# Performance work log

Measured on AMD Instinct MI355X. Metric: run time of the kernel, lower is better.

## Reference

```python
import jax, jax.numpy as jnp
import numpy as np

B, C, LO, LQ, H = 64, 4, 64, 128, 768
NEG = -10000.0


def _trilinear(u, um, v, vm, w1, b1, w2, b2, w3):
    # u: [N, Lu, H], v: [N, Lv, H]; returns [N, Lu, Lv]
    p1 = u @ w1 + b1                                  # [N, Lu, 1]
    p2 = (v @ w2 + b2).transpose(0, 2, 1)             # [N, 1, Lv]
    p3 = jnp.einsum('bud,bvd->buv', u * w3, v)        # trilinear term
    return p1 + p2 + p3 + ((1.0 - um) * NEG)[:, :, None] + ((1.0 - vm) * NEG)[:, None, :]


def _forward(encoded_o, encoded_q, om, qm,
             att_W1_w, att_W1_b, att_W2_w, att_W2_b, att_W3,
             Wc_self_w, Wc_self_b, Wc_w, Wc_b, Va_w, Va_b, Wg_w, Wg_b,
             co_W1_w, co_W1_b, co_W2_w, co_W2_b, co_W3, Wp_w, Wp_b,
             sa_W1_w, sa_W1_b, sa_W2_w, sa_W2_b, sa_W3, Wf_w, Wf_b):
    b, c, lo, h = encoded_o.shape
    lq = encoded_q.shape[2]
    p = c * (c - 1)
    # ---- pairwise option-compare (OCN_Att_layer) over all (i, j), j != i ----
    i_idx = np.repeat(np.arange(c), c - 1)
    j_idx = np.array([j for i in range(c) for j in range(c) if j != i])
    o_i = encoded_o[:, i_idx].reshape(b * p, lo, h)   # 'ok'
    o_j = encoded_o[:, j_idx].reshape(b * p, lo, h)   # 'ol'
    m_i = om[:, i_idx].reshape(b * p, lo)
    m_j = om[:, j_idx].reshape(b * p, lo)
    A = _trilinear(o_j, m_j, o_i, m_i, att_W1_w, att_W1_b, att_W2_w, att_W2_b, att_W3)
    att = jax.nn.softmax(A, axis=1)
    olk_ctx = jnp.einsum('bud,buv->bvd', o_j, att)    # [BP, LO, H]
    OLK = jnp.concatenate([o_i - olk_ctx, o_i * olk_ctx], axis=-1)  # [BP, LO, 2H]
    cmp_proj = OLK @ Wc_w + Wc_b                      # Wc applied per compare pair
    cmp_sum = cmp_proj.reshape(b, c, c - 1, lo, h).sum(axis=2).reshape(b * c, lo, h)
    # ---- merge layer (per candidate, flattened into batch) ----
    o1 = encoded_o.reshape(b * c, lo, h)
    q = encoded_q.reshape(b * c, lq, h)
    omf = om.reshape(b * c, lo)
    qmf = qm.reshape(b * c, lq)
    Aq = jax.nn.softmax(q @ Va_w + Va_b + ((1.0 - qmf) * NEG)[:, :, None], axis=1)  # [BC, LQ, 1]
    Q = jnp.einsum('bld,blo->bod', q, Aq)             # [BC, 1, H]
    OCK = jnp.tanh(o1 @ Wc_self_w + Wc_self_b + cmp_sum)
    Qb = jnp.broadcast_to(Q, (b * c, lo, h))
    G = jax.nn.sigmoid(jnp.concatenate([o1, OCK, Qb], axis=-1) @ Wg_w + Wg_b)
    merged = G * o1 + (1.0 - G) * OCK                 # [BC, LO, H]
    # ---- co-attention with question ----
    A2 = _trilinear(q, qmf, merged, omf, co_W1_w, co_W1_b, co_W2_w, co_W2_b, co_W3)  # [BC, LQ, LO]
    ACK = jax.nn.softmax(A2, axis=2)
    OA = jnp.einsum('bqo,bod->bqd', ACK, merged)      # [BC, LQ, H]
    APK = jax.nn.softmax(A2, axis=1)
    dOA = jnp.concatenate([q, OA], axis=-1)           # [BC, LQ, 2H]
    POAA = jnp.einsum('bqd,bqo->bod', dOA, APK)       # [BC, LO, 2H]
    OPK = jax.nn.relu(jnp.concatenate([merged, POAA], axis=-1) @ Wp_w + Wp_b)
    # ---- self-attention ----
    A3 = _trilinear(OPK, omf, OPK, omf, sa_W1_w, sa_W1_b, sa_W2_w, sa_W2_b, sa_W3)
    att3 = jax.nn.softmax(A3, axis=1)
    OSK = jnp.einsum('bud,buv->bvd', OPK, att3)
    OFK = jax.nn.relu(jnp.concatenate([OPK, OSK, OPK - OSK, OPK * OSK], axis=-1) @ Wf_w + Wf_b)
    return OFK.reshape(b, c, lo, h).max(axis=2)       # [B, C, H]


def setup_inputs():
    ks = jax.random.split(jax.random.key(0), 32)
    def p(i, shape, s=0.02):
        return jax.random.normal(ks[i], shape, jnp.float32) * s
    return {
        'encoded_o': jax.random.normal(ks[0], (B, C, LO, H), jnp.float32),
        'encoded_q': jax.random.normal(ks[1], (B, C, LQ, H), jnp.float32),
        'option_mask': jnp.ones((B, C, LO), jnp.int32),
        'question_mask': jnp.ones((B, C, LQ), jnp.int32),
        'att_W1_w': p(2, (H, 1)), 'att_W1_b': p(3, (1,)),
        'att_W2_w': p(4, (H, 1)), 'att_W2_b': p(5, (1,)),
        'att_W3': p(6, (H,)),
        'Wc_self_w': p(7, (H, H)), 'Wc_self_b': p(8, (H,)),
        'Wc_w': p(9, (2 * H, H)), 'Wc_b': p(10, (H,)),
        'Va_w': p(11, (H, 1)), 'Va_b': p(12, (1,)),
        'Wg_w': p(13, (3 * H, H)), 'Wg_b': p(14, (H,)),
        'co_W1_w': p(15, (H, 1)), 'co_W1_b': p(16, (1,)),
        'co_W2_w': p(17, (H, 1)), 'co_W2_b': p(18, (1,)),
        'co_W3': p(19, (H,)),
        'Wp_w': p(20, (3 * H, H)), 'Wp_b': p(21, (H,)),
        'sa_W1_w': p(22, (H, 1)), 'sa_W1_b': p(23, (1,)),
        'sa_W2_w': p(24, (H, 1)), 'sa_W2_b': p(25, (1,)),
        'sa_W3': p(26, (H,)),
        'Wf_w': p(27, (4 * H, H)), 'Wf_b': p(28, (H,)),
    }


def reference(encoded_o, encoded_q, option_mask, question_mask,
              att_W1_w, att_W1_b, att_W2_w, att_W2_b, att_W3,
              Wc_self_w, Wc_self_b, Wc_w, Wc_b, Va_w, Va_b, Wg_w, Wg_b,
              co_W1_w, co_W1_b, co_W2_w, co_W2_b, co_W3, Wp_w, Wp_b,
              sa_W1_w, sa_W1_b, sa_W2_w, sa_W2_b, sa_W3, Wf_w, Wf_b):
    return _forward(encoded_o, encoded_q,
                    option_mask.astype(jnp.float32), question_mask.astype(jnp.float32),
                    att_W1_w, att_W1_b, att_W2_w, att_W2_b, att_W3,
                    Wc_self_w, Wc_self_b, Wc_w, Wc_b, Va_w, Va_b, Wg_w, Wg_b,
                    co_W1_w, co_W1_b, co_W2_w, co_W2_b, co_W3, Wp_w, Wp_b,
                    sa_W1_w, sa_W1_b, sa_W2_w, sa_W2_b, sa_W3, Wf_w, Wf_b)
```

## Files before the change

kernel.cpp:

```cpp
#include <hip/hip_runtime.h>
#include <math.h>


#define NEGC (-10000.0f)
constexpr int HD = 768;

constexpr int EP_TANH = 1;
constexpr int EP_MERGE = 2;
constexpr int EP_RELU = 3;
constexpr int EP_RELU_MAX = 4;

typedef __attribute__((ext_vector_type(8))) short bf16x8;
typedef __attribute__((ext_vector_type(8))) unsigned short u16x8;
typedef __attribute__((ext_vector_type(4))) unsigned short u16x4;
typedef __attribute__((ext_vector_type(4))) float f32x4;

__device__ inline void st8(float* dst, float4 a0, float4 a1) {
  dst[0] = a0.x; dst[1] = a0.y; dst[2] = a0.z; dst[3] = a0.w;
  dst[4] = a1.x; dst[5] = a1.y; dst[6] = a1.z; dst[7] = a1.w;
}

__device__ inline unsigned short f2bf(float x) {
  unsigned int u = __float_as_uint(x);
  u += 0x7fffu + ((u >> 16) & 1u);
  return (unsigned short)(u >> 16);
}

__device__ inline float bf2f(unsigned short u) {
  return __uint_as_float(((unsigned int)u) << 16);
}

__device__ inline u16x8 pack8(float4 a, float4 b) {
  u16x8 r;
  r[0] = f2bf(a.x); r[1] = f2bf(a.y); r[2] = f2bf(a.z); r[3] = f2bf(a.w);
  r[4] = f2bf(b.x); r[5] = f2bf(b.y); r[6] = f2bf(b.z); r[7] = f2bf(b.w);
  return r;
}

// ... 54 lines not shown
                    float* __restrict__ o1, float* __restrict__ o2, int ntok) {
  int tok = blockIdx.x * 4 + (threadIdx.x >> 6);
  int lane = threadIdx.x & 63;
  if (tok >= ntok) return;
  const unsigned short* xp = x + (size_t)tok * HD;
  unsigned short* xw = xw3 + (size_t)tok * HD;
  float s1 = 0.f, s2 = 0.f;
#pragma unroll
  for (int i = 0; i < 3; ++i) {
    int c = (lane + (i << 6)) << 2;
    u16x4 xv = *(const u16x4*)(xp + c);
    float x0 = bf2f(xv[0]), x1 = bf2f(xv[1]), x2 = bf2f(xv[2]), x3 = bf2f(xv[3]);
    float4 w3v = *(const float4*)(w3 + c);
    float4 wa = *(const float4*)(w1 + c);
    float4 wb = *(const float4*)(w2 + c);
    s1 = fmaf(x0, wa.x, s1); s1 = fmaf(x1, wa.y, s1);
    s1 = fmaf(x2, wa.z, s1); s1 = fmaf(x3, wa.w, s1);
    s2 = fmaf(x0, wb.x, s2); s2 = fmaf(x1, wb.y, s2);
    s2 = fmaf(x2, wb.z, s2); s2 = fmaf(x3, wb.w, s2);
    u16x4 sv;
    sv[0] = f2bf(x0 * w3v.x); sv[1] = f2bf(x1 * w3v.y);
    sv[2] = f2bf(x2 * w3v.z); sv[3] = f2bf(x3 * w3v.w);
    *(u16x4*)(xw + c) = sv;
  }
#pragma unroll
  for (int off = 32; off; off >>= 1) {
    s1 += __shfl_xor(s1, off);
    s2 += __shfl_xor(s2, off);
  }
  if (lane == 0) { o1[tok] = s1 + b1[0]; o2[tok] = s2 + b2[0]; }
}

__global__ __launch_bounds__(256)
void dot768x2_f32(const float* __restrict__ x,
                  const float* __restrict__ w1, const float* __restrict__ b1,
                  const float* __restrict__ w2, const float* __restrict__ b2,
                  float* __restrict__ o1, float* __restrict__ o2, int ntok) {
  int tok = blockIdx.x * 4 + (threadIdx.x >> 6);
  int lane = threadIdx.x & 63;
  if (tok >= ntok) return;
  const float* xp = x + (size_t)tok * HD;
  float s1 = 0.f, s2 = 0.f;
#pragma unroll
  for (int i = 0; i < 3; ++i) {
    int c = (lane + (i << 6)) << 2;
    float4 xv = *(const float4*)(xp + c);
    float4 wa = *(const float4*)(w1 + c);
    float4 wb = *(const float4*)(w2 + c);
    s1 = fmaf(xv.x, wa.x, s1); s1 = fmaf(xv.y, wa.y, s1);
    s1 = fmaf(xv.z, wa.z, s1); s1 = fmaf(xv.w, wa.w, s1);
    s2 = fmaf(xv.x, wb.x, s2); s2 = fmaf(xv.y, wb.y, s2);
    s2 = fmaf(xv.z, wb.z, s2); s2 = fmaf(xv.w, wb.w, s2);
  }
#pragma unroll
  for (int off = 32; off; off >>= 1) {
    s1 += __shfl_xor(s1, off);
    s2 += __shfl_xor(s2, off);
  }
  if (lane == 0) { o1[tok] = s1 + b1[0]; o2[tok] = s2 + b2[0]; }
}

__global__ __launch_bounds__(256)
void dot768_bf16(const unsigned short* __restrict__ x,
                 const float* __restrict__ w1, const float* __restrict__ b1,
                 float* __restrict__ o1, int ntok) {
  int tok = blockIdx.x * 4 + (threadIdx.x >> 6);
  int lane = threadIdx.x & 63;
  if (tok >= ntok) return;
  const unsigned short* xp = x + (size_t)tok * HD;
  float s1 = 0.f;
#pragma unroll
  for (int i = 0; i < 3; ++i) {
    int c = (lane + (i << 6)) << 2;
    u16x4 xv = *(const u16x4*)(xp + c);
    float4 wa = *(const float4*)(w1 + c);
    s1 = fmaf(bf2f(xv[0]), wa.x, s1); s1 = fmaf(bf2f(xv[1]), wa.y, s1);
    s1 = fmaf(bf2f(xv[2]), wa.z, s1); s1 = fmaf(bf2f(xv[3]), wa.w, s1);
  }
#pragma unroll
  for (int off = 32; off; off >>= 1) s1 += __shfl_xor(s1, off);
  if (lane == 0) o1[tok] = s1 + b1[0];
}

__global__ void bias_ock_kernel(const float* __restrict__ b1, const float* __restrict__ b2,
                                float* __restrict__ o) {
  int n = blockIdx.x * 256 + threadIdx.x;
  if (n < HD) o[n] = b1[n] + 3.f * b2[n];
}

template<int NJ>
__global__ __launch_bounds__(256)
void p1_kernel(const unsigned short* __restrict__ Xbf, const unsigned short* __restrict__ Xw3,
               const float* __restrict__ s1g, const float* __restrict__ s2g,
               const int* __restrict__ maskg, unsigned short* __restrict__ PtG) {
  __shared__ __align__(16) unsigned short Ua[64 * 136];
  __shared__ __align__(16) unsigned short Vb[64 * 136];
  __shared__ float Sbuf[64][66];
  __shared__ float red[4][64];
  const int t = threadIdx.x;
  int ubc, vbc;
  if (NJ == 1) {
    ubc = vbc = blockIdx.x;
  } else {
    const int b = blockIdx.x / 12, pr = blockIdx.x % 12;
    const int i = pr / 3, jj = pr % 3;
    const int j = jj + (jj >= i ? 1 : 0);
    vbc = (b << 2) + i; ubc = (b << 2) + j;
  }
  const unsigned short* U = Xbf + (size_t)ubc * (64 * HD);
  const unsigned short* V = Xw3 + (size_t)vbc * (64 * HD);
  const int w = t >> 6, lane = t & 63, l15 = lane & 15, l4 = lane >> 4;
  const int srow = t >> 2, scol = (t & 3) << 5;
  f32x4 acc[4] = {};
  for (int k0 = 0; k0 < HD; k0 += 128) {
    const unsigned short* up = U + (size_t)srow * HD + k0 + scol;
    const unsigned short* vp = V + (size_t)srow * HD + k0 + scol;
    unsigned short* ua = &Ua[srow * 136 + scol];
    unsigned short* vb = &Vb[srow * 136 + scol];
#pragma unroll
    for (int z = 0; z < 4; ++z) {
// ... 110 lines not shown
        bf16x8 af = *(const bf16x8*)(ptj + (m * 16 + l15) * 72 + ks * 32 + l4 * 8);
#pragma unroll
        for (int n = 0; n < 3; ++n)
          acc[m][n] = __builtin_amdgcn_mfma_f32_16x16x32_bf16(af, bfr[n], acc[m][n], 0, 0, 0);
      }
    }
  }
  const unsigned short* oip = Oi + (size_t)bc * (64 * HD);
  const size_t obase = (size_t)bc * (64 * HD);
#pragma unroll
  for (int m = 0; m < 4; ++m)
#pragma unroll
    for (int n = 0; n < 3; ++n) {
      const int d = d0 + (w * 3 + n) * 16 + l15;
#pragma unroll
      for (int r = 0; r < 4; ++r) {
        const int v = m * 16 + l4 * 4 + r;
        const size_t idx = obase + (size_t)v * HD + d;
        const float cs = acc[m][n][r];
        const float oi = bf2f(oip[(size_t)v * HD + d]);
        if (NJ == 3) {
          y1[idx] = f2bf(fmaf(3.f, oi, -cs));
          y2[idx] = f2bf(oi * cs);
        } else {
          osk[idx] = f2bf(cs);
          y1[idx] = f2bf(oi - cs);
          y2[idx] = f2bf(oi * cs);
        }
      }
    }
}

__global__ __launch_bounds__(256)
void qpool_kernel(const float* __restrict__ q, const float* __restrict__ qa,
                  const int* __restrict__ qm, float* __restrict__ Q) {
  __shared__ float wgt[128];
  __shared__ float wred[4];
  int t = threadIdx.x, bc = blockIdx.x;
  const float* qap = qa + bc * 128;
  const int* qmp = qm + bc * 128;
  float v = -1e30f;
  if (t < 128) v = qap[t] + (1.f - (float)qmp[t]) * NEGC;
  float m = v;
#pragma unroll
  for (int off = 32; off; off >>= 1) m = fmaxf(m, __shfl_xor(m, off));
  if ((t & 63) == 0) wred[t >> 6] = m;
  __syncthreads();
  float gm = fmaxf(fmaxf(wred[0], wred[1]), fmaxf(wred[2], wred[3]));
  float e = (t < 128) ? expf(v - gm) : 0.f;
  float s = e;
#pragma unroll
  for (int off = 32; off; off >>= 1) s += __shfl_xor(s, off);
  __syncthreads();
  if ((t & 63) == 0) wred[t >> 6] = s;
  __syncthreads();
  float tot = wred[0] + wred[1] + wred[2] + wred[3];
  if (t < 128) wgt[t] = e / tot;
  __syncthreads();
  const float* qp = q + (size_t)bc * (128 * HD);
  float* Qp = Q + (size_t)bc * HD;
  for (int d = t; d < HD; d += 256) {
    float acc = 0.f;
    for (int l = 0; l < 128; ++l) acc = fmaf(wgt[l], qp[(size_t)l * HD + d], acc);
    Qp[d] = acc;
  }
}

__global__ __launch_bounds__(256)
void a2_mfma_kernel(const float* __restrict__ qin, const unsigned short* __restrict__ mergedb,
                    const float* __restrict__ qco1, const float* __restrict__ ms2,
                    const int* __restrict__ qm, const int* __restrict__ om,
                    const float* __restrict__ w3, float* __restrict__ A2) {
  __shared__ __align__(16) unsigned short Aq[64 * 72];
  __shared__ __align__(16) unsigned short Bm[64 * 72];
  const int t = threadIdx.x, qh = blockIdx.x, bc = blockIdx.y;
  const float* qp = qin + (size_t)bc * (128 * HD) + (size_t)(qh * 64) * HD;
  const unsigned short* mp = mergedb + (size_t)bc * (64 * HD);
  const int w = t >> 6, lane = t & 63, l15 = lane & 15, l4 = lane >> 4;
  const int srow = t >> 2, scs = (t & 3) << 4;
  f32x4 acc[4] = {};
  for (int k0 = 0; k0 < HD; k0 += 64) {
    {
      const float* p = qp + (size_t)srow * HD + k0 + scs;
      const float* wp = w3 + k0 + scs;
      unsigned short* dst = &Aq[srow * 72 + scs];
#pragma unroll
      for (int z = 0; z < 2; ++z) {
        float4 a = *(const float4*)(p + z * 8);
        float4 b = *(const float4*)(p + z * 8 + 4);
        float4 wa = *(const float4*)(wp + z * 8);
        float4 wb = *(const float4*)(wp + z * 8 + 4);
        a.x *= wa.x; a.y *= wa.y; a.z *= wa.z; a.w *= wa.w;
        b.x *= wb.x; b.y *= wb.y; b.z *= wb.z; b.w *= wb.w;
        *(u16x8*)(dst + z * 8) = pack8(a, b);
      }
    }
    {
      const unsigned short* p = mp + (size_t)srow * HD + k0 + scs;
      unsigned short* dst = &Bm[srow * 72 + scs];
      *(u16x8*)(dst) = *(const u16x8*)(p);
      *(u16x8*)(dst + 8) = *(const u16x8*)(p + 8);
    }
    __syncthreads();
#pragma unroll
    for (int ks = 0; ks < 2; ++ks) {
      bf16x8 af = *(const bf16x8*)(&Aq[(w * 16 + l15) * 72 + ks * 32 + l4 * 8]);
#pragma unroll
      for (int n = 0; n < 4; ++n) {
        bf16x8 bf = *(const bf16x8*)(&Bm[(n * 16 + l15) * 72 + ks * 32 + l4 * 8]);
        acc[n] = __builtin_amdgcn_mfma_f32_16x16x32_bf16(af, bf, acc[n], 0, 0, 0);
      }
    }
    __syncthreads();
  }
  const float* qc = qco1 + bc * 128;
  const int* qmp = qm + bc * 128;
  const float* msp = ms2 + bc * 64;
  const int* omp = om + bc * 64;
  float* outp = A2 + (size_t)bc * (128 * 64) + (size_t)(qh * 64) * 64;
#pragma unroll
  for (int n = 0; n < 4; ++n) {
    const int v = n * 16 + l15;
    const float ct = msp[v] + (1.f - (float)omp[v]) * NEGC;
#pragma unroll
    for (int r = 0; r < 4; ++r) {
      const int ql = w * 16 + l4 * 4 + r;
      const int qrow = qh * 64 + ql;
      const float rt = qc[qrow] + (1.f - (float)qmp[qrow]) * NEGC;
      outp[ql * 64 + v] = acc[n][r] + rt + ct;
    }
  }
}

__global__ __launch_bounds__(256)
void poaa_mfma_kernel(const float* __restrict__ A2, const float* __restrict__ qin,
                      const unsigned short* __restrict__ mergedb,
                      unsigned short* __restrict__ PLO, unsigned short* __restrict__ PHI) {
  __shared__ __align__(16) char smem[77312];
  __shared__ float red[4][64];
  __shared__ float rowm[128], rowfac[128];
  __shared__ float colfac[64];
  __shared__ float gmax_s;
  float* T = (float*)smem;
  unsigned short* Tt = (unsigned short*)(smem + 33280);
  unsigned short* Tft = (unsigned short*)(smem + 50688);
  unsigned short* M2bf = (unsigned short*)(smem + 68096);
  unsigned short* Qc = (unsigned short*)smem;
  unsigned short* Mc = (unsigned short*)(smem + 18432);

  const int t = threadIdx.x, dqh = blockIdx.x, bc = blockIdx.y;
  const int w = t >> 6, lane = t & 63, l15 = lane & 15, l4 = lane >> 4;
  const float* a2 = A2 + (size_t)bc * (128 * 64);
  {
    int row = t >> 1, cs = (t & 1) << 5;
    const float* p = a2 + row * 64 + cs;
#pragma unroll
    for (int z = 0; z < 8; ++z) {
      float4 v = *(const float4*)(p + (z << 2));
      T[row * 65 + cs + (z << 2) + 0] = v.x;
      T[row * 65 + cs + (z << 2) + 1] = v.y;
      T[row * 65 + cs + (z << 2) + 2] = v.z;
      T[row * 65 + cs + (z << 2) + 3] = v.w;
    }
  }
  __syncthreads();
  {
    int qrow = t >> 1, h = t & 1;
    float m = -1e30f;
    for (int v = h * 32; v < h * 32 + 32; ++v) m = fmaxf(m, T[qrow * 65 + v]);
    m = fmaxf(m, __shfl_xor(m, 1));
    float s = 0.f;
    for (int v = h * 32; v < h * 32 + 32; ++v) s += expf(T[qrow * 65 + v] - m);
    s += __shfl_xor(s, 1);
    if (h == 0) { rowm[qrow] = m; rowfac[qrow] = s; }
  }
  float colm_loc = 0.f;
  {
    int v = t & 63, part = t >> 6;
    float m = -1e30f;
    for (int qq = part * 32; qq < part * 32 + 32; ++qq) m = fmaxf(m, T[qq * 65 + v]);
    red[part][v] = m;
    __syncthreads();
    float cm = fmaxf(fmaxf(red[0][v], red[1][v]), fmaxf(red[2][v], red[3][v]));
    float s = 0.f;
    for (int qq = part * 32; qq < part * 32 + 32; ++qq) s += expf(T[qq * 65 + v] - cm);
    __syncthreads();
    red[part][v] = s;
    __syncthreads();
    if (part == 0) { colm_loc = cm; colfac[v] = red[0][v] + red[1][v] + red[2][v] + red[3][v]; }
  }
  __syncthreads();
  if (t < 64) {
    float m = fmaxf(rowm[t], rowm[t + 64]);
#pragma unroll
    for (int off = 32; off; off >>= 1) m = fmaxf(m, __shfl_xor(m, off));
// ... 9 lines not shown
    for (int z = 0; z < 32; ++z) {
      const int qq = qs + z;
      float e = expf(T[qq * 65 + o] - gmax);
      Tt[o * 136 + qq] = f2bf(e);
      Tft[o * 136 + qq] = f2bf(e * rowfac[qq]);
    }
  }
  __syncthreads();
  {
    f32x4 m2acc[4] = {};
#pragma unroll
    for (int ks = 0; ks < 4; ++ks) {
      bf16x8 af = *(const bf16x8*)(&Tt[(w * 16 + l15) * 136 + ks * 32 + l4 * 8]);
#pragma unroll
      for (int n = 0; n < 4; ++n) {
        bf16x8 bf = *(const bf16x8*)(&Tft[(n * 16 + l15) * 136 + ks * 32 + l4 * 8]);
        m2acc[n] = __builtin_amdgcn_mfma_f32_16x16x32_bf16(af, bf, m2acc[n], 0, 0, 0);
      }
    }
#pragma unroll
    for (int n = 0; n < 4; ++n)
#pragma unroll
      for (int r = 0; r < 4; ++r) {
        const int o = w * 16 + l4 * 4 + r;
        M2bf[o * 72 + n * 16 + l15] = f2bf(colfac[o] * m2acc[n][r]);
      }
  }
  const int dql = t >> 1, dqs = (t & 1) << 5;
  const int dml = t >> 2, dms = (t & 3) << 4;
  const int swq = ((dql >> 3) & 3) << 5;
  const int swm = ((dml >> 3) & 3) << 5;
  unsigned short* plo = PLO + (size_t)bc * (64 * HD);
  unsigned short* phi = PHI + (size_t)bc * (64 * HD);
  const float* qp = qin + (size_t)bc * (128 * HD);
  const unsigned short* mp = mergedb + (size_t)bc * (64 * HD);
  for (int dc = dqh * 6; dc < dqh * 6 + 6; ++dc) {
    const int d0 = dc * 64;
    __syncthreads();
    {
      const float* p = qp + (size_t)dql * HD + d0 + dqs;
#pragma unroll
      for (int z = 0; z < 4; ++z) {
        float4 a = *(const float4*)(p + z * 8);
        float4 b = *(const float4*)(p + z * 8 + 4);
        *(u16x8*)((char*)Qc + ((dql * 144 + (dqs + z * 8) * 2) ^ swq)) = pack8(a, b);
      }
    }
    {
      const unsigned short* p = mp + (size_t)dml * HD + d0 + dms;
      *(u16x8*)((char*)Mc + ((dml * 144 + dms * 2) ^ swm)) = *(const u16x8*)p;
      *(u16x8*)((char*)Mc + ((dml * 144 + (dms + 8) * 2) ^ swm)) = *(const u16x8*)(p + 8);
    }
    __syncthreads();
    const int col = w * 16 + l15;
    f32x4 lacc[4] = {};
#pragma unroll
    for (int ks = 0; ks < 4; ++ks) {
      bf16x8 bf;
#pragma unroll
      for (int e = 0; e < 8; ++e) {
        const int qq = ks * 32 + l4 * 8 + e;
        bf[e] = *(const short*)((const char*)Qc + ((qq * 144 + col * 2) ^ (((qq >> 3) & 3) << 5)));
      }
#pragma unroll
      for (int m = 0; m < 4; ++m) {
        bf16x8 af = *(const bf16x8*)(&Tt[(m * 16 + l15) * 136 + ks * 32 + l4 * 8]);
        lacc[m] = __builtin_amdgcn_mfma_f32_16x16x32_bf16(af, bf, lacc[m], 0, 0, 0);
      }
// ... 54 lines not shown
      float4 a0 = *(const float4*)(Ap + k0);
      float4 a1 = *(const float4*)(Ap + k0 + 4);
      st8(&As[arow][acs], a0, a1);
      float4 w0 = *(const float4*)(Wp + (size_t)k0 * HD);
      float4 w1 = *(const float4*)(Wp + (size_t)k0 * HD + 4);
      st8(&Ws[wrow][wcs], w0, w1);
      __syncthreads();
#pragma unroll
      for (int kk = 0; kk < 32; ++kk) {
        float av[4], bv[4];
#pragma unroll
        for (int x = 0; x < 4; ++x) av[x] = As[(tr << 2) + x][kk];
#pragma unroll
        for (int y = 0; y < 4; ++y) bv[y] = Ws[kk][(tc << 2) + y];
#pragma unroll
        for (int x = 0; x < 4; ++x)
#pragma unroll
          for (int y = 0; y < 4; ++y) acc[x][y] = fmaf(av[x], bv[y], acc[x][y]);
      }
      __syncthreads();
    }
  }
#pragma unroll
  for (int x = 0; x < 4; ++x) {
    const int r = m0 + (tr << 2) + x;
#pragma unroll
    for (int y = 0; y < 4; ++y) {
      const int n = n0 + (tc << 2) + y;
      g.out[(size_t)r * HD + n] = acc[x][y] + g.bias[n];
    }
  }
}

struct WcArgs {
  const float* src[4];
  unsigned short* dst;
  int Kw;
};

__global__ __launch_bounds__(256)
void wconv_kernel(WcArgs g) {
  __shared__ float tile[64][65];
  const int slice = blockIdx.y;
  const float* src = g.src[slice];
  const int kbase = slice * HD;
  const int bi = blockIdx.x % 12, bj = blockIdx.x / 12;
  const int t = threadIdx.x;
  const int r = t >> 2, cseg = (t & 3) << 4;
  const float* p = src + (size_t)(bi * 64 + r) * HD + bj * 64 + cseg;
#pragma unroll
  for (int j = 0; j < 16; j += 4) {
    float4 v = *(const float4*)(p + j);
    tile[r][cseg + j + 0] = v.x; tile[r][cseg + j + 1] = v.y;
    tile[r][cseg + j + 2] = v.z; tile[r][cseg + j + 3] = v.w;
  }
  __syncthreads();
  unsigned short* q = g.dst + (size_t)(bj * 64 + r) * g.Kw + kbase + bi * 64 + cseg;
  u16x8 lo, hi;
#pragma unroll
  for (int j = 0; j < 8; ++j) lo[j] = f2bf(tile[cseg + j][r]);
#pragma unroll
  for (int j = 0; j < 8; ++j) hi[j] = f2bf(tile[cseg + 8 + j][r]);
  *(u16x8*)q = lo;
  *(u16x8*)(q + 8) = hi;
}

struct MMArgs {
  const unsigned short* a[4];
  int K;
  const unsigned short* wt;
  const float* bias;
  const unsigned short* aux0;
  const unsigned short* aux1;
  const float* aux2;
  float* outf;
  unsigned short* outb;
};

template<int EP>
__global__ __launch_bounds__(256)
void mfma_gemm_kernel(MMArgs g) {
  __shared__ __align__(16) unsigned short As[3][128 * 32];
  __shared__ __align__(16) unsigned short Bs[3][128 * 32];
  const int t = threadIdx.x;
  const int lane = t & 63, w = t >> 6;
  const int wr = w >> 1, wc = w & 1;
  const int m0 = blockIdx.x << 7, n0 = blockIdx.y << 7;
  const int l15 = lane & 15, l4 = lane >> 4;
  f32x4 acc[4][4] = {};

  const int srow = w * 32 + (lane >> 2);
  const int gcol = (((lane & 3) ^ ((lane >> 3) & 3))) * 8;
  const int rsw = (l15 >> 1) & 3;
  const int rcol = ((l4 ^ rsw)) * 8;

  const int nkt = g.K >> 5;

  auto issue = [&](int kt, int buf) {
    const int c = kt / 24;
    const int koff = (kt - c * 24) << 5;
    const unsigned short* ap = g.a[c] + (size_t)(m0 + srow) * HD + koff + gcol;
    const unsigned short* bp = g.wt + (size_t)(n0 + srow) * g.K + (kt << 5) + gcol;
    gload_lds16(ap, &As[buf][w * 1024]);
    gload_lds16(ap + (size_t)16 * HD, &As[buf][w * 1024 + 512]);
    gload_lds16(bp, &Bs[buf][w * 1024]);
    gload_lds16(bp + (size_t)16 * g.K, &Bs[buf][w * 1024 + 512]);
  };

  auto compute = [&](int kt, int buf, bool prefetch) {
    bf16x8 af[4], bfr[4];
#pragma unroll
    for (int mi = 0; mi < 4; ++mi)
      af[mi] = *(const bf16x8*)(&As[buf][(wr * 64 + mi * 16 + l15) * 32 + rcol]);
#pragma unroll
    for (int ni = 0; ni < 4; ++ni)
      bfr[ni] = *(const bf16x8*)(&Bs[buf][(wc * 64 + ni * 16 + l15) * 32 + rcol]);
    asm volatile("s_waitcnt lgkmcnt(0)" ::: "memory");
    __builtin_amdgcn_s_barrier();
    if (prefetch) issue(kt + 3, buf);
#pragma unroll
    for (int mi = 0; mi < 4; ++mi)
#pragma unroll
      for (int ni = 0; ni < 4; ++ni)
        acc[mi][ni] = __builtin_amdgcn_mfma_f32_16x16x32_bf16(af[mi], bfr[ni], acc[mi][ni], 0, 0, 0);
  };

  issue(0, 0); issue(1, 1); issue(2, 2);
  int buf = 0;
  int kt = 0;
  for (; kt < nkt - 2; ++kt) {
    asm volatile("s_waitcnt vmcnt(8)" ::: "memory");
    __builtin_amdgcn_s_barrier();
    compute(kt, buf, kt + 3 < nkt);
    buf = (buf == 2) ? 0 : buf + 1;
  }
  asm volatile("s_waitcnt vmcnt(4)" ::: "memory");
  __builtin_amdgcn_s_barrier();
  compute(kt, buf, false);
  buf = (buf == 2) ? 0 : buf + 1;
  ++kt;
  asm volatile("s_waitcnt vmcnt(0)" ::: "memory");
  __builtin_amdgcn_s_barrier();
  compute(kt, buf, false);

  if (EP == EP_RELU_MAX) {
#pragma unroll
    for (int ni = 0; ni < 4; ++ni) {
      const int n = n0 + wc * 64 + ni * 16 + l15;
      const float b = g.bias[n];
      float m = 0.f;
#pragma unroll
      for (int mi = 0; mi < 4; ++mi)
#pragma unroll
        for (int r = 0; r < 4; ++r)
          m = fmaxf(m, acc[mi][ni][r] + b);
      m = fmaxf(m, 0.f);
      m = fmaxf(m, __shfl_xor(m, 16));
// ... 34 lines not shown
  const float* enc_q = (const float*)d_in[1];
  const int* om = (const int*)d_in[2];
  const int* qm = (const int*)d_in[3];
  const float* att_W1_w = (const float*)d_in[4];
  const float* att_W1_b = (const float*)d_in[5];
  const float* att_W2_w = (const float*)d_in[6];
  const float* att_W2_b = (const float*)d_in[7];
  const float* att_W3 = (const float*)d_in[8];
  const float* Wc_self_w = (const float*)d_in[9];
  const float* Wc_self_b = (const float*)d_in[10];
  const float* Wc_w = (const float*)d_in[11];
  const float* Wc_b = (const float*)d_in[12];
  const float* Va_w = (const float*)d_in[13];
  const float* Va_b = (const float*)d_in[14];
  const float* Wg_w = (const float*)d_in[15];
  const float* Wg_b = (const float*)d_in[16];
  const float* co_W1_w = (const float*)d_in[17];
  const float* co_W1_b = (const float*)d_in[18];
  const float* co_W2_w = (const float*)d_in[19];
  const float* co_W2_b = (const float*)d_in[20];
  const float* co_W3 = (const float*)d_in[21];
  const float* Wp_w = (const float*)d_in[22];
  const float* Wp_b = (const float*)d_in[23];
  const float* sa_W1_w = (const float*)d_in[24];
  const float* sa_W1_b = (const float*)d_in[25];
  const float* sa_W2_w = (const float*)d_in[26];
  const float* sa_W2_b = (const float*)d_in[27];
  const float* sa_W3 = (const float*)d_in[28];
  const float* Wf_w = (const float*)d_in[29];
  const float* Wf_b = (const float*)d_in[30];
  float* out = (float*)d_out;

  const int NTOK_O = 16384;
  const int NTOK_Q = 32768;
  const int HH = 768 * 768;

  float* ws = (float*)d_ws;
  size_t off = 0;
  auto carve = [&](size_t n) { float* p = ws + off; off += n; return p; };
  float* s1o   = carve(16384);
  float* s2o   = carve(16384);
  float* qa    = carve(32768);
  float* qco1  = carve(32768);
  float* ms2   = carve(16384);
  float* sa1   = carve(16384);
  float* sa2   = carve(16384);
  float* biasO = carve(1024);
  float* Qpool = carve(196608);
  float* Qg    = carve(196608);
  float* A2buf = carve(2097152);
  float* r1 = carve(12582912);
  float* r2 = carve(12582912);
  float* r3 = carve(12582912);
  float* r4 = carve(12582912);
  unsigned short* wtb = (unsigned short*)carve(1179648);
  if (ws_size < off * sizeof(float)) return;
  unsigned short* OPKb  = (unsigned short*)r1;
  unsigned short* X1    = (unsigned short*)(r1 + 6291456);
  unsigned short* X3    = (unsigned short*)(r1 + 6291456);
  unsigned short* OCKb  = (unsigned short*)r2;
  unsigned short* PLOb  = (unsigned short*)r2;
  unsigned short* opkw3 = (unsigned short*)r2;
  unsigned short* X2    = (unsigned short*)(r2 + 6291456);
  unsigned short* MRGb  = (unsigned short*)r3;
  unsigned short* OSKb  = (unsigned short*)r3;
  unsigned short* X4    = (unsigned short*)(r3 + 6291456);
  unsigned short* eobf  = (unsigned short*)r4;
  unsigned short* eow3  = (unsigned short*)(r4 + 6291456);
  unsigned short* PHIb  = (unsigned short*)r4;
  unsigned short* PtG   = (unsigned short*)A2buf;

  const dim3 GBIG(128, 6);

  bfprep_dot_kernel<<<NTOK_O / 4, 256, 0, stream>>>(enc_o, att_W3, att_W1_w, att_W1_b,
                                                    att_W2_w, att_W2_b, eobf, eow3,
                                                    s1o, s2o, NTOK_O);
  dot768x2_f32<<<NTOK_Q / 4, 256, 0, stream>>>(enc_q, Va_w, Va_b,
                                               co_W1_w, co_W1_b, qa, qco1, NTOK_Q);
  bias_ock_kernel<<<3, 256, 0, stream>>>(Wc_self_b, Wc_b, biasO);

  p1_kernel<3><<<768, 256, 0, stream>>>(eobf, eow3, s1o, s2o, om, PtG);
  p2_kernel<3><<<dim3(4, 256), 256, 0, stream>>>(eobf, PtG, eobf, nullptr, X1, X2);

  {
    WcArgs wa{};
    wa.src[0] = Wc_self_w; wa.src[1] = Wc_w; wa.src[2] = Wc_w + HH;
    wa.dst = wtb; wa.Kw = 2304;
    wconv_kernel<<<dim3(144, 3), 256, 0, stream>>>(wa);
    MMArgs g{};
    g.a[0] = eobf; g.a[1] = X1; g.a[2] = X2;
    g.K = 2304; g.wt = wtb; g.bias = biasO; g.outb = OCKb;
    mfma_gemm_kernel<EP_TANH><<<GBIG, 256, 0, stream>>>(g);
  }

  qpool_kernel<<<256, 256, 0, stream>>>(enc_q, qa, qm, Qpool);
  {
    GemmArgs g{};
    g.a[0] = Qpool; g.w[0] = Wg_w + 2 * HH;
    g.nchunks = 1; g.bias = Wg_b; g.out = Qg;
    gemm_store_kernel<<<dim3(12, 4), 256, 0, stream>>>(g);
  }

  {
    WcArgs wa{};
    wa.src[0] = Wg_w; wa.src[1] = Wg_w + HH;
    wa.dst = wtb; wa.Kw = 1536;
    wconv_kernel<<<dim3(144, 2), 256, 0, stream>>>(wa);
    MMArgs g{};
    g.a[0] = eobf; g.a[1] = OCKb;
    g.K = 1536; g.wt = wtb; g.bias = nullptr;
    g.aux0 = eobf; g.aux1 = OCKb; g.aux2 = Qg; g.outb = MRGb;
    mfma_gemm_kernel<EP_MERGE><<<GBIG, 256, 0, stream>>>(g);
  }

  dot768_bf16<<<NTOK_O / 4, 256, 0, stream>>>(MRGb, co_W2_w, co_W2_b, ms2, NTOK_O);
  a2_mfma_kernel<<<dim3(2, 256), 256, 0, stream>>>(enc_q, MRGb, qco1, ms2, qm, om, co_W3, A2buf);
  poaa_mfma_kernel<<<dim3(2, 256), 256, 0, stream>>>(A2buf, enc_q, MRGb, PLOb, PHIb);

  {
    WcArgs wa{};
    wa.src[0] = Wp_w; wa.src[1] = Wp_w + HH; wa.src[2] = Wp_w + 2 * HH;
    wa.dst = wtb; wa.Kw = 2304;
    wconv_kernel<<<dim3(144, 3), 256, 0, stream>>>(wa);
    MMArgs g{};
    g.a[0] = MRGb; g.a[1] = PLOb; g.a[2] = PHIb;
    g.K = 2304; g.wt = wtb; g.bias = Wp_b; g.outb = OPKb;
    mfma_gemm_kernel<EP_RELU><<<GBIG, 256, 0, stream>>>(g);
  }

  opkprep_kernel<<<NTOK_O / 4, 256, 0, stream>>>(OPKb, sa_W3, sa_W1_w, sa_W1_b,
                                                 sa_W2_w, sa_W2_b, opkw3, sa1, sa2, NTOK_O);
  p1_kernel<1><<<256, 256, 0, stream>>>(OPKb, opkw3, sa1, sa2, om, PtG);
  p2_kernel<1><<<dim3(4, 256), 256, 0, stream>>>(OPKb, PtG, OPKb, OSKb, X3, X4);

  {
    WcArgs wa{};
    wa.src[0] = Wf_w; wa.src[1] = Wf_w + HH; wa.src[2] = Wf_w + 2 * HH; wa.src[3] = Wf_w + 3 * HH;
    wa.dst = wtb; wa.Kw = 3072;
    wconv_kernel<<<dim3(144, 4), 256, 0, stream>>>(wa);
    MMArgs g{};
    g.a[0] = OPKb; g.a[1] = OSKb; g.a[2] = X3; g.a[3] = X4;
    g.K = 3072; g.wt = wtb; g.bias = Wf_b; g.outf = out;
    mfma_gemm_kernel<EP_RELU_MAX><<<GBIG, 256, 0, stream>>>(g);
  }
}
```

Before: 619.7 us.

## Fuse q projections into qpool, fold A2 into poaa, batch weight conversion

Merges the q-token dot products (Va and co_W1) into the qpool kernel, which removes one launch and a separate pass over enc_q. Folds the A2 trilinear MFMA computation into the poaa kernel so A2 no longer round-trips through global memory. Converts all twelve weight slices to bf16 in a single launch into one wide-stride buffer, replacing four separate conversions. It also adds s_setprio around the GEMM MFMA loop. The trade-offs are less parallelism in qpool (256 blocks, each doing 128 token dots serially), each poaa block now recomputing the full 128-row A2, and the wide weight buffer reusing part of the r4 scratch region.

```diff
diff --git a/kernel.cpp b/kernel.cpp
--- a/kernel.cpp
+++ b/kernel.cpp
@@ -4,6 +4,7 @@
 
 #define NEGC (-10000.0f)
 constexpr int HD = 768;
+constexpr int KSTR = 9216;
 
 constexpr int EP_TANH = 1;
 constexpr int EP_MERGE = 2;
@@ -124,35 +125,6 @@
 }
 
 __global__ __launch_bounds__(256)
-void dot768x2_f32(const float* __restrict__ x,
-                  const float* __restrict__ w1, const float* __restrict__ b1,
-                  const float* __restrict__ w2, const float* __restrict__ b2,
-                  float* __restrict__ o1, float* __restrict__ o2, int ntok) {
-  int tok = blockIdx.x * 4 + (threadIdx.x >> 6);
-  int lane = threadIdx.x & 63;
-  if (tok >= ntok) return;
-  const float* xp = x + (size_t)tok * HD;
-  float s1 = 0.f, s2 = 0.f;
-#pragma unroll
-  for (int i = 0; i < 3; ++i) {
-    int c = (lane + (i << 6)) << 2;
-    float4 xv = *(const float4*)(xp + c);
-    float4 wa = *(const float4*)(w1 + c);
-    float4 wb = *(const float4*)(w2 + c);
-    s1 = fmaf(xv.x, wa.x, s1); s1 = fmaf(xv.y, wa.y, s1);
-    s1 = fmaf(xv.z, wa.z, s1); s1 = fmaf(xv.w, wa.w, s1);
-    s2 = fmaf(xv.x, wb.x, s2); s2 = fmaf(xv.y, wb.y, s2);
-    s2 = fmaf(xv.z, wb.z, s2); s2 = fmaf(xv.w, wb.w, s2);
-  }
-#pragma unroll
-  for (int off = 32; off; off >>= 1) {
-    s1 += __shfl_xor(s1, off);
-    s2 += __shfl_xor(s2, off);
-  }
-  if (lane == 0) { o1[tok] = s1 + b1[0]; o2[tok] = s2 + b2[0]; }
-}
-
-__global__ __launch_bounds__(256)
 void dot768_bf16(const unsigned short* __restrict__ x,
                  const float* __restrict__ w1, const float* __restrict__ b1,
                  float* __restrict__ o1, int ntok) {
@@ -178,6 +150,71 @@
                                 float* __restrict__ o) {
   int n = blockIdx.x * 256 + threadIdx.x;
   if (n < HD) o[n] = b1[n] + 3.f * b2[n];
+}
+
+__global__ __launch_bounds__(256)
+void qpool2_kernel(const float* __restrict__ q,
+                   const float* __restrict__ Va_w, const float* __restrict__ Va_b,
+                   const float* __restrict__ coW1_w, const float* __restrict__ coW1_b,
+                   const int* __restrict__ qm,
+                   float* __restrict__ qco1, float* __restrict__ Q) {
+  __shared__ float qa_s[128];
+  __shared__ float wgt[128];
+  __shared__ float wred[4];
+  const int t = threadIdx.x, bc = blockIdx.x;
+  const int lane = t & 63, wv = t >> 6;
+  const float* qb = q + (size_t)bc * (128 * HD);
+  for (int it = 0; it < 32; ++it) {
+    const int tl = it * 4 + wv;
+    const float* xp = qb + (size_t)tl * HD;
+    float s1 = 0.f, s2 = 0.f;
+#pragma unroll
+    for (int i = 0; i < 3; ++i) {
+      int c = (lane + (i << 6)) << 2;
+      float4 xv = *(const float4*)(xp + c);
+      float4 wa = *(const float4*)(Va_w + c);
+      float4 wb = *(const float4*)(coW1_w + c);
+      s1 = fmaf(xv.x, wa.x, s1); s1 = fmaf(xv.y, wa.y, s1);
+      s1 = fmaf(xv.z, wa.z, s1); s1 = fmaf(xv.w, wa.w, s1);
+      s2 = fmaf(xv.x, wb.x, s2); s2 = fmaf(xv.y, wb.y, s2);
+      s2 = fmaf(xv.z, wb.z, s2); s2 = fmaf(xv.w, wb.w, s2);
+    }
+#pragma unroll
+    for (int off = 32; off; off >>= 1) {
+      s1 += __shfl_xor(s1, off);
+      s2 += __shfl_xor(s2, off);
+    }
+    if (lane == 0) {
+      qa_s[tl] = s1 + Va_b[0];
+      qco1[bc * 128 + tl] = s2 + coW1_b[0];
+    }
+  }
+  __syncthreads();
+  const int* qmp = qm + bc * 128;
+  float v = -1e30f;
+  if (t < 128) v = qa_s[t] + (1.f - (float)qmp[t]) * NEGC;
+  float m = v;
+#pragma unroll
+  for (int off = 32; off; off >>= 1) m = fmaxf(m, __shfl_xor(m, off));
+  if ((t & 63) == 0) wred[t >> 6] = m;
+  __syncthreads();
+  float gm = fmaxf(fmaxf(wred[0], wred[1]), fmaxf(wred[2], wred[3]));
+  float e = (t < 128) ? expf(v - gm) : 0.f;
+  float s = e;
+#pragma unroll
+  for (int off = 32; off; off >>= 1) s += __shfl_xor(s, off);
+  __syncthreads();
+  if ((t & 63) == 0) wred[t >> 6] = s;
+  __syncthreads();
+  float tot = wred[0] + wred[1] + wred[2] + wred[3];
+  if (t < 128) wgt[t] = e / tot;
+  __syncthreads();
+  float* Qp = Q + (size_t)bc * HD;
+  for (int d = t; d < HD; d += 256) {
+    float acc = 0.f;
+    for (int l = 0; l < 128; ++l) acc = fmaf(wgt[l], qb[(size_t)l * HD + d], acc);
+    Qp[d] = acc;
+  }
 }
 
 template<int NJ>
@@ -354,116 +391,19 @@
 }
 
 __global__ __launch_bounds__(256)
-void qpool_kernel(const float* __restrict__ q, const float* __restrict__ qa,
-                  const int* __restrict__ qm, float* __restrict__ Q) {
-  __shared__ float wgt[128];
-  __shared__ float wred[4];
-  int t = threadIdx.x, bc = blockIdx.x;
-  const float* qap = qa + bc * 128;
-  const int* qmp = qm + bc * 128;
-  float v = -1e30f;
-  if (t < 128) v = qap[t] + (1.f - (float)qmp[t]) * NEGC;
-  float m = v;
-#pragma unroll
-  for (int off = 32; off; off >>= 1) m = fmaxf(m, __shfl_xor(m, off));
-  if ((t & 63) == 0) wred[t >> 6] = m;
-  __syncthreads();
-  float gm = fmaxf(fmaxf(wred[0], wred[1]), fmaxf(wred[2], wred[3]));
-  float e = (t < 128) ? expf(v - gm) : 0.f;
-  float s = e;
-#pragma unroll
-  for (int off = 32; off; off >>= 1) s += __shfl_xor(s, off);
-  __syncthreads();
-  if ((t & 63) == 0) wred[t >> 6] = s;
-  __syncthreads();
-  float tot = wred[0] + wred[1] + wred[2] + wred[3];
-  if (t < 128) wgt[t] = e / tot;
-  __syncthreads();
-  const float* qp = q + (size_t)bc * (128 * HD);
-  float* Qp = Q + (size_t)bc * HD;
-  for (int d = t; d < HD; d += 256) {
-    float acc = 0.f;
-    for (int l = 0; l < 128; ++l) acc = fmaf(wgt[l], qp[(size_t)l * HD + d], acc);
-    Qp[d] = acc;
-  }
-}
-
-__global__ __launch_bounds__(256)
-void a2_mfma_kernel(const float* __restrict__ qin, const unsigned short* __restrict__ mergedb,
-                    const float* __restrict__ qco1, const float* __restrict__ ms2,
-                    const int* __restrict__ qm, const int* __restrict__ om,
-                    const float* __restrict__ w3, float* __restrict__ A2) {
-  __shared__ __align__(16) unsigned short Aq[64 * 72];
-  __shared__ __align__(16) unsigned short Bm[64 * 72];
-  const int t = threadIdx.x, qh = blockIdx.x, bc = blockIdx.y;
-  const float* qp = qin + (size_t)bc * (128 * HD) + (size_t)(qh * 64) * HD;
-  const unsigned short* mp = mergedb + (size_t)bc * (64 * HD);
-  const int w = t >> 6, lane = t & 63, l15 = lane & 15, l4 = lane >> 4;
-  const int srow = t >> 2, scs = (t & 3) << 4;
-  f32x4 acc[4] = {};
-  for (int k0 = 0; k0 < HD; k0 += 64) {
-    {
-      const float* p = qp + (size_t)srow * HD + k0 + scs;
-      const float* wp = w3 + k0 + scs;
-      unsigned short* dst = &Aq[srow * 72 + scs];
-#pragma unroll
-      for (int z = 0; z < 2; ++z) {
-        float4 a = *(const float4*)(p + z * 8);
-        float4 b = *(const float4*)(p + z * 8 + 4);
-        float4 wa = *(const float4*)(wp + z * 8);
-        float4 wb = *(const float4*)(wp + z * 8 + 4);
-        a.x *= wa.x; a.y *= wa.y; a.z *= wa.z; a.w *= wa.w;
-        b.x *= wb.x; b.y *= wb.y; b.z *= wb.z; b.w *= wb.w;
-        *(u16x8*)(dst + z * 8) = pack8(a, b);
-      }
-    }
-    {
-      const unsigned short* p = mp + (size_t)srow * HD + k0 + scs;
-      unsigned short* dst = &Bm[srow * 72 + scs];
-      *(u16x8*)(dst) = *(const u16x8*)(p);
-      *(u16x8*)(dst + 8) = *(const u16x8*)(p + 8);
-    }
-    __syncthreads();
-#pragma unroll
-    for (int ks = 0; ks < 2; ++ks) {
-      bf16x8 af = *(const bf16x8*)(&Aq[(w * 16 + l15) * 72 + ks * 32 + l4 * 8]);
-#pragma unroll
-      for (int n = 0; n < 4; ++n) {
-        bf16x8 bf = *(const bf16x8*)(&Bm[(n * 16 + l15) * 72 + ks * 32 + l4 * 8]);
-        acc[n] = __builtin_amdgcn_mfma_f32_16x16x32_bf16(af, bf, acc[n], 0, 0, 0);
-      }
-    }
-    __syncthreads();
-  }
-  const float* qc = qco1 + bc * 128;
-  const int* qmp = qm + bc * 128;
-  const float* msp = ms2 + bc * 64;
-  const int* omp = om + bc * 64;
-  float* outp = A2 + (size_t)bc * (128 * 64) + (size_t)(qh * 64) * 64;
-#pragma unroll
-  for (int n = 0; n < 4; ++n) {
-    const int v = n * 16 + l15;
-    const float ct = msp[v] + (1.f - (float)omp[v]) * NEGC;
-#pragma unroll
-    for (int r = 0; r < 4; ++r) {
-      const int ql = w * 16 + l4 * 4 + r;
-      const int qrow = qh * 64 + ql;
-      const float rt = qc[qrow] + (1.f - (float)qmp[qrow]) * NEGC;
-      outp[ql * 64 + v] = acc[n][r] + rt + ct;
-    }
-  }
-}
-
-__global__ __launch_bounds__(256)
-void poaa_mfma_kernel(const float* __restrict__ A2, const float* __restrict__ qin,
-                      const unsigned short* __restrict__ mergedb,
-                      unsigned short* __restrict__ PLO, unsigned short* __restrict__ PHI) {
+void poaa2_kernel(const float* __restrict__ qin, const unsigned short* __restrict__ mergedb,
+                  const float* __restrict__ qco1, const float* __restrict__ ms2,
+                  const int* __restrict__ qm, const int* __restrict__ om,
+                  const float* __restrict__ w3,
+                  unsigned short* __restrict__ PLO, unsigned short* __restrict__ PHI) {
   __shared__ __align__(16) char smem[77312];
   __shared__ float red[4][64];
   __shared__ float rowm[128], rowfac[128];
   __shared__ float colfac[64];
   __shared__ float gmax_s;
   float* T = (float*)smem;
+  unsigned short* Aq = (unsigned short*)smem;
+  unsigned short* Bm = (unsigned short*)(smem + 18432);
   unsigned short* Tt = (unsigned short*)(smem + 33280);
   unsigned short* Tft = (unsigned short*)(smem + 50688);
   unsigned short* M2bf = (unsigned short*)(smem + 68096);
@@ -472,17 +412,69 @@
 
   const int t = threadIdx.x, dqh = blockIdx.x, bc = blockIdx.y;
   const int w = t >> 6, lane = t & 63, l15 = lane & 15, l4 = lane >> 4;
-  const float* a2 = A2 + (size_t)bc * (128 * 64);
-  {
-    int row = t >> 1, cs = (t & 1) << 5;
-    const float* p = a2 + row * 64 + cs;
-#pragma unroll
-    for (int z = 0; z < 8; ++z) {
-      float4 v = *(const float4*)(p + (z << 2));
-      T[row * 65 + cs + (z << 2) + 0] = v.x;
-      T[row * 65 + cs + (z << 2) + 1] = v.y;
-      T[row * 65 + cs + (z << 2) + 2] = v.z;
-      T[row * 65 + cs + (z << 2) + 3] = v.w;
+  const float* qp = qin + (size_t)bc * (128 * HD);
+  const unsigned short* mp = mergedb + (size_t)bc * (64 * HD);
+  const float* qc = qco1 + bc * 128;
+  const int* qmp = qm + bc * 128;
+  const float* msp = ms2 + bc * 64;
+  const int* omp = om + bc * 64;
+
+  {
+    const int arow = t >> 1, acs = (t & 1) << 5;
+    const int brow = t >> 2, bcs = (t & 3) << 4;
+    f32x4 acc[2][4] = {};
+    for (int k0 = 0; k0 < HD; k0 += 64) {
+      {
+        const float* p = qp + (size_t)arow * HD + k0 + acs;
+        const float* wp = w3 + k0 + acs;
+        unsigned short* dst = &Aq[arow * 72 + acs];
+#pragma unroll
+        for (int z = 0; z < 4; ++z) {
+          float4 a = *(const float4*)(p + z * 8);
+          float4 b = *(const float4*)(p + z * 8 + 4);
+          float4 wa = *(const float4*)(wp + z * 8);
+          float4 wb = *(const float4*)(wp + z * 8 + 4);
+          a.x *= wa.x; a.y *= wa.y; a.z *= wa.z; a.w *= wa.w;
+          b.x *= wb.x; b.y *= wb.y; b.z *= wb.z; b.w *= wb.w;
+          *(u16x8*)(dst + z * 8) = pack8(a, b);
+        }
+      }
+      {
+        const unsigned short* p = mp + (size_t)brow * HD + k0 + bcs;
+        unsigned short* dst = &Bm[brow * 72 + bcs];
+        *(u16x8*)(dst) = *(const u16x8*)(p);
+        *(u16x8*)(dst + 8) = *(const u16x8*)(p + 8);
+      }
+      __syncthreads();
+#pragma unroll
+      for (int ks = 0; ks < 2; ++ks) {
+        bf16x8 af[2], bf[4];
+#pragma unroll
+        for (int m = 0; m < 2; ++m)
+          af[m] = *(const bf16x8*)(&Aq[(w * 32 + m * 16 + l15) * 72 + ks * 32 + l4 * 8]);
+#pragma unroll
+        for (int n = 0; n < 4; ++n)
+          bf[n] = *(const bf16x8*)(&Bm[(n * 16 + l15) * 72 + ks * 32 + l4 * 8]);
+#pragma unroll
+        for (int m = 0; m < 2; ++m)
+#pragma unroll
+          for (int n = 0; n < 4; ++n)
+            acc[m][n] = __builtin_amdgcn_mfma_f32_16x16x32_bf16(af[m], bf[n], acc[m][n], 0, 0, 0);
+      }
+      __syncthreads();
+    }
+#pragma unroll
+    for (int n = 0; n < 4; ++n) {
+      const int v = n * 16 + l15;
+      const float ct = msp[v] + (1.f - (float)omp[v]) * NEGC;
+#pragma unroll
+      for (int m = 0; m < 2; ++m)
+#pragma unroll
+        for (int r = 0; r < 4; ++r) {
+          const int qrow = w * 32 + m * 16 + l4 * 4 + r;
+          const float rt = qc[qrow] + (1.f - (float)qmp[qrow]) * NEGC;
+          T[qrow * 65 + v] = acc[m][n][r] + rt + ct;
+        }
     }
   }
   __syncthreads();
@@ -558,8 +550,6 @@
   const int swm = ((dml >> 3) & 3) << 5;
   unsigned short* plo = PLO + (size_t)bc * (64 * HD);
   unsigned short* phi = PHI + (size_t)bc * (64 * HD);
-  const float* qp = qin + (size_t)bc * (128 * HD);
-  const unsigned short* mp = mergedb + (size_t)bc * (64 * HD);
   for (int dc = dqh * 6; dc < dqh * 6 + 6; ++dc) {
     const int d0 = dc * 64;
     __syncthreads();
@@ -680,18 +670,17 @@
   }
 }
 
-struct WcArgs {
-  const float* src[4];
+struct WcAllArgs {
+  const float* src[12];
+  int basecol[12];
   unsigned short* dst;
-  int Kw;
 };
 
 __global__ __launch_bounds__(256)
-void wconv_kernel(WcArgs g) {
+void wconv_all_kernel(WcAllArgs g) {
   __shared__ float tile[64][65];
   const int slice = blockIdx.y;
   const float* src = g.src[slice];
-  const int kbase = slice * HD;
   const int bi = blockIdx.x % 12, bj = blockIdx.x / 12;
   const int t = threadIdx.x;
   const int r = t >> 2, cseg = (t & 3) << 4;
@@ -703,7 +692,7 @@
     tile[r][cseg + j + 2] = v.z; tile[r][cseg + j + 3] = v.w;
   }
   __syncthreads();
-  unsigned short* q = g.dst + (size_t)(bj * 64 + r) * g.Kw + kbase + bi * 64 + cseg;
+  unsigned short* q = g.dst + (size_t)(bj * 64 + r) * KSTR + g.basecol[slice] + bi * 64 + cseg;
   u16x8 lo, hi;
 #pragma unroll
   for (int j = 0; j < 8; ++j) lo[j] = f2bf(tile[cseg + j][r]);
@@ -748,11 +737,11 @@
     const int c = kt / 24;
     const int koff = (kt - c * 24) << 5;
     const unsigned short* ap = g.a[c] + (size_t)(m0 + srow) * HD + koff + gcol;
-    const unsigned short* bp = g.wt + (size_t)(n0 + srow) * g.K + (kt << 5) + gcol;
+    const unsigned short* bp = g.wt + (size_t)(n0 + srow) * KSTR + (kt << 5) + gcol;
     gload_lds16(ap, &As[buf][w * 1024]);
     gload_lds16(ap + (size_t)16 * HD, &As[buf][w * 1024 + 512]);
     gload_lds16(bp, &Bs[buf][w * 1024]);
-    gload_lds16(bp + (size_t)16 * g.K, &Bs[buf][w * 1024 + 512]);
+    gload_lds16(bp + (size_t)16 * KSTR, &Bs[buf][w * 1024 + 512]);
   };
 
   auto compute = [&](int kt, int buf, bool prefetch) {
@@ -766,11 +755,13 @@
     asm volatile("s_waitcnt lgkmcnt(0)" ::: "memory");
     __builtin_amdgcn_s_barrier();
     if (prefetch) issue(kt + 3, buf);
+    __builtin_amdgcn_s_setprio(1);
 #pragma unroll
     for (int mi = 0; mi < 4; ++mi)
 #pragma unroll
       for (int ni = 0; ni < 4; ++ni)
         acc[mi][ni] = __builtin_amdgcn_mfma_f32_16x16x32_bf16(af[mi], bfr[ni], acc[mi][ni], 0, 0, 0);
+    __builtin_amdgcn_s_setprio(0);
   };
 
   issue(0, 0); issue(1, 1); issue(2, 2);
@@ -871,7 +862,6 @@
   float* out = (float*)d_out;
 
   const int NTOK_O = 16384;
-  const int NTOK_Q = 32768;
   const int HH = 768 * 768;
 
   float* ws = (float*)d_ws;
@@ -879,7 +869,6 @@
   auto carve = [&](size_t n) { float* p = ws + off; off += n; return p; };
   float* s1o   = carve(16384);
   float* s2o   = carve(16384);
-  float* qa    = carve(32768);
   float* qco1  = carve(32768);
   float* ms2   = carve(16384);
   float* sa1   = carve(16384);
@@ -892,7 +881,6 @@
   float* r2 = carve(12582912);
   float* r3 = carve(12582912);
   float* r4 = carve(12582912);
-  unsigned short* wtb = (unsigned short*)carve(1179648);
   if (ws_size < off * sizeof(float)) return;
   unsigned short* OPKb  = (unsigned short*)r1;
   unsigned short* X1    = (unsigned short*)(r1 + 6291456);
@@ -907,6 +895,7 @@
   unsigned short* eobf  = (unsigned short*)r4;
   unsigned short* eow3  = (unsigned short*)(r4 + 6291456);
   unsigned short* PHIb  = (unsigned short*)r4;
+  unsigned short* wall  = (unsigned short*)(r4 + 6291456);
   unsigned short* PtG   = (unsigned short*)A2buf;
 
   const dim3 GBIG(128, 6);
@@ -914,25 +903,32 @@
   bfprep_dot_kernel<<<NTOK_O / 4, 256, 0, stream>>>(enc_o, att_W3, att_W1_w, att_W1_b,
                                                     att_W2_w, att_W2_b, eobf, eow3,
                                                     s1o, s2o, NTOK_O);
-  dot768x2_f32<<<NTOK_Q / 4, 256, 0, stream>>>(enc_q, Va_w, Va_b,
-                                               co_W1_w, co_W1_b, qa, qco1, NTOK_Q);
+  qpool2_kernel<<<256, 256, 0, stream>>>(enc_q, Va_w, Va_b, co_W1_w, co_W1_b,
+                                         qm, qco1, Qpool);
   bias_ock_kernel<<<3, 256, 0, stream>>>(Wc_self_b, Wc_b, biasO);
 
   p1_kernel<3><<<768, 256, 0, stream>>>(eobf, eow3, s1o, s2o, om, PtG);
+  {
+    WcAllArgs wa{};
+    wa.src[0] = Wc_self_w; wa.src[1] = Wc_w;        wa.src[2] = Wc_w + HH;
+    wa.src[3] = Wg_w;      wa.src[4] = Wg_w + HH;
+    wa.src[5] = Wp_w;      wa.src[6] = Wp_w + HH;   wa.src[7] = Wp_w + 2 * HH;
+    wa.src[8] = Wf_w;      wa.src[9] = Wf_w + HH;   wa.src[10] = Wf_w + 2 * HH;
+    wa.src[11] = Wf_w + 3 * HH;
+    int bases[12] = {0, 768, 1536, 2304, 3072, 3840, 4608, 5376, 6144, 6912, 7680, 8448};
+    for (int i = 0; i < 12; ++i) wa.basecol[i] = bases[i];
+    wa.dst = wall;
+    wconv_all_kernel<<<dim3(144, 12), 256, 0, stream>>>(wa);
+  }
   p2_kernel<3><<<dim3(4, 256), 256, 0, stream>>>(eobf, PtG, eobf, nullptr, X1, X2);
 
   {
-    WcArgs wa{};
-    wa.src[0] = Wc_self_w; wa.src[1] = Wc_w; wa.src[2] = Wc_w + HH;
-    wa.dst = wtb; wa.Kw = 2304;
-    wconv_kernel<<<dim3(144, 3), 256, 0, stream>>>(wa);
     MMArgs g{};
     g.a[0] = eobf; g.a[1] = X1; g.a[2] = X2;
-    g.K = 2304; g.wt = wtb; g.bias = biasO; g.outb = OCKb;
+    g.K = 2304; g.wt = wall + 0; g.bias = biasO; g.outb = OCKb;
     mfma_gemm_kernel<EP_TANH><<<GBIG, 256, 0, stream>>>(g);
   }
 
-  qpool_kernel<<<256, 256, 0, stream>>>(enc_q, qa, qm, Qpool);
   {
     GemmArgs g{};
     g.a[0] = Qpool; g.w[0] = Wg_w + 2 * HH;
@@ -941,29 +937,21 @@
   }
 
   {
-    WcArgs wa{};
-    wa.src[0] = Wg_w; wa.src[1] = Wg_w + HH;
-    wa.dst = wtb; wa.Kw = 1536;
-    wconv_kernel<<<dim3(144, 2), 256, 0, stream>>>(wa);
     MMArgs g{};
     g.a[0] = eobf; g.a[1] = OCKb;
-    g.K = 1536; g.wt = wtb; g.bias = nullptr;
+    g.K = 1536; g.wt = wall + 2304; g.bias = nullptr;
     g.aux0 = eobf; g.aux1 = OCKb; g.aux2 = Qg; g.outb = MRGb;
     mfma_gemm_kernel<EP_MERGE><<<GBIG, 256, 0, stream>>>(g);
   }
 
   dot768_bf16<<<NTOK_O / 4, 256, 0, stream>>>(MRGb, co_W2_w, co_W2_b, ms2, NTOK_O);
-  a2_mfma_kernel<<<dim3(2, 256), 256, 0, stream>>>(enc_q, MRGb, qco1, ms2, qm, om, co_W3, A2buf);
-  poaa_mfma_kernel<<<dim3(2, 256), 256, 0, stream>>>(A2buf, enc_q, MRGb, PLOb, PHIb);
-
-  {
-    WcArgs wa{};
-    wa.src[0] = Wp_w; wa.src[1] = Wp_w + HH; wa.src[2] = Wp_w + 2 * HH;
-    wa.dst = wtb; wa.Kw = 2304;
-    wconv_kernel<<<dim3(144, 3), 256, 0, stream>>>(wa);
+  poaa2_kernel<<<dim3(2, 256), 256, 0, stream>>>(enc_q, MRGb, qco1, ms2, qm, om,
+                                                 co_W3, PLOb, PHIb);
+
+  {
     MMArgs g{};
     g.a[0] = MRGb; g.a[1] = PLOb; g.a[2] = PHIb;
-    g.K = 2304; g.wt = wtb; g.bias = Wp_b; g.outb = OPKb;
+    g.K = 2304; g.wt = wall + 3840; g.bias = Wp_b; g.outb = OPKb;
     mfma_gemm_kernel<EP_RELU><<<GBIG, 256, 0, stream>>>(g);
   }
 
@@ -973,13 +961,9 @@
   p2_kernel<1><<<dim3(4, 256), 256, 0, stream>>>(OPKb, PtG, OPKb, OSKb, X3, X4);
 
   {
-    WcArgs wa{};
-    wa.src[0] = Wf_w; wa.src[1] = Wf_w + HH; wa.src[2] = Wf_w + 2 * HH; wa.src[3] = Wf_w + 3 * HH;
-    wa.dst = wtb; wa.Kw = 3072;
-    wconv_kernel<<<dim3(144, 4), 256, 0, stream>>>(wa);
     MMArgs g{};
     g.a[0] = OPKb; g.a[1] = OSKb; g.a[2] = X3; g.a[3] = X4;
-    g.K = 3072; g.wt = wtb; g.bias = Wf_b; g.outf = out;
+    g.K = 3072; g.wt = wall + 6144; g.bias = Wf_b; g.outf = out;
     mfma_gemm_kernel<EP_RELU_MAX><<<GBIG, 256, 0, stream>>>(g);
   }
 }
```

Result: no change. 609.4 us (-1.7%).
